# Performance work log

Hardware: AMD Instinct MI355X
Metric: run time of the kernel (lower is better)

Reference implementation:

```python
import jax, jax.numpy as jnp
import numpy as np

B, T, C, H = 8, 2048, 768, 768

def setup_inputs() -> dict:
    key = jax.random.key(0)
    ks = jax.random.split(key, 7)
    s = 1.0 / np.sqrt(C)
    return {
        "visual_token": jax.random.normal(ks[0], (B, T, C), dtype=jnp.float32),
        "Wk": jax.random.normal(ks[1], (H, C), dtype=jnp.float32) * s,
        "bk": jax.random.normal(ks[2], (H,), dtype=jnp.float32) * s,
        "Wq": jax.random.normal(ks[3], (H, C), dtype=jnp.float32) * s,
        "bq": jax.random.normal(ks[4], (H,), dtype=jnp.float32) * s,
        "W1": jax.random.normal(ks[5], (C, C), dtype=jnp.float32) * s,
        "W2": jax.random.normal(ks[6], (C, C), dtype=jnp.float32) * s,
    }

def reference(visual_token, Wk, bk, Wq, bq, W1, W2):
    x = visual_token
    k = jnp.einsum('btc,hc->bth', x, Wk) + bk          # [B,T,H]
    q = jnp.einsum('btc,hc->bth', x, Wq) + bq          # [B,T,H]
    scores = jnp.einsum('bih,bjh->bij', k, q)          # K @ Q^T, unscaled
    attn = jax.nn.softmax(scores, axis=1)              # NOTE: softmax over dim=1 as in source
    p = x + jnp.einsum('bij,bjc->bic', attn, x)        # residual with value = input
    h = jnp.einsum('btc,dc->btd', p, W1)               # f_1 (no bias)
    h = jnp.einsum('btd,ed->bte', h, W2)               # f_2 (no bias)
    return p + jax.nn.relu(h)
```

## Files before the change

kernel.cpp:

```cpp
#include <hip/hip_runtime.h>

typedef float    f32x4 __attribute__((ext_vector_type(4)));
typedef _Float16 f16x8 __attribute__((ext_vector_type(8)));
typedef _Float16 f16x4 __attribute__((ext_vector_type(4)));

__device__ __forceinline__ void gload16(const void* g, void* l) {
  __builtin_amdgcn_global_load_lds(
      (__attribute__((address_space(1))) void*)(const void*)g,
      (__attribute__((address_space(3))) void*)l,
      16, 0, 0);
}

template <int EPI>
__global__ __launch_bounds__(512, 4) void gemm_kt(
    const _Float16* __restrict__ A, size_t sA, int lda,
    const _Float16* __restrict__ B, size_t sB, int ldb,
    float* __restrict__ out0, _Float16* __restrict__ out1,
    float* __restrict__ out2,
    size_t sO, int ldo,
    const float* __restrict__ bias,
    const float* __restrict__ resid,
    const _Float16* __restrict__ residh,
    const _Float16* __restrict__ cf,
    int K) {
  __shared__ _Float16 lds[3 * 12288];
  __shared__ _Float16 clds[(EPI == 6) ? 4096 : 1];

  const int gx = gridDim.x, gy = gridDim.y;
  const int nblk = gx * gy * gridDim.z;
  int lin = (blockIdx.z * gy + blockIdx.y) * gx + blockIdx.x;
  lin = (lin & 7) * (nblk >> 3) + (lin >> 3);
  const int b  = lin / (gx * gy);
  const int r2 = lin - b * gx * gy;
  const int m0 = (r2 / gx) * 128;
  const int n0 = (r2 - (r2 / gx) * gx) * 256;

  const int t = threadIdx.x, lane = t & 63, w = t >> 6;
  const int wr = w >> 2;
  const int wc = w & 3;
  const int lr = lane & 15, lq = lane >> 4;

  const _Float16* Ab = A + (size_t)b * sA;
  const _Float16* Bb = B + (size_t)b * sB;

  const int arow = t >> 2;
  const int acol = ((t & 3) ^ ((arow >> 1) & 3)) * 8;
  const _Float16* a_src  = Ab + (size_t)(m0 + arow) * lda + acol;
  const _Float16* b_src0 = Bb + (size_t)(n0 + arow) * ldb + acol;
  const _Float16* b_src1 = b_src0 + (size_t)128 * ldb;
  const int a_dst  = t * 8;
  const int b_dst0 = 4096 + t * 8;
  const int b_dst1 = 4096 + (t + 512) * 8;

  const int swz  = ((lr >> 1) & 3) << 3;
  const int koff = (lq * 8) ^ swz;
  const int a_rd = (wr * 64 + lr) * 32 + koff;
  const int b_rd = 4096 + (wc * 64 + lr) * 32 + koff;

  f32x4 acc[4][4];
#pragma unroll
  for (int f = 0; f < 4; ++f)
#pragma unroll
    for (int j = 0; j < 4; ++j) acc[f][j] = (f32x4){0.f, 0.f, 0.f, 0.f};

  const int NT = K >> 5;

  if constexpr (EPI == 6)
    gload16(cf + ((size_t)b * 32 + (m0 >> 6)) * 2048 + t * 8, clds + t * 8);
  gload16(a_src,       lds + a_dst);
  gload16(b_src0,      lds + b_dst0);
  gload16(b_src1,      lds + b_dst1);
  gload16(a_src  + 32, lds + 12288 + a_dst);
  gload16(b_src0 + 32, lds + 12288 + b_dst0);
  gload16(b_src1 + 32, lds + 12288 + b_dst1);

  int buf = 0;
  for (int kt = 0; kt < NT; ++kt) {
    if (kt + 1 < NT) asm volatile("s_waitcnt vmcnt(3)" ::: "memory");
    else             asm volatile("s_waitcnt vmcnt(0)" ::: "memory");
    __builtin_amdgcn_s_barrier();
    __builtin_amdgcn_sched_barrier(0);

    const _Float16* lb = lds + buf * 12288;
    const int nb = (buf + 2 >= 3) ? buf - 1 : buf + 2;
    _Float16* ln = lds + nb * 12288;

    f16x8 af[4], bf[4], cv;
    if constexpr (EPI == 6)
      cv = *(const f16x8*)(clds + wr * 2048 + kt * 32 + lq * 8);
#pragma unroll
    for (int f = 0; f < 4; ++f) {
      af[f] = *(const f16x8*)(lb + a_rd + f * 512);
      if constexpr (EPI == 6) af[f] = af[f] * cv;
    }
#pragma unroll
    for (int j = 0; j < 4; ++j) bf[j] = *(const f16x8*)(lb + b_rd + j * 512);
    if (kt + 2 < NT) {
      const int ko = (kt + 2) * 32;
      gload16(a_src  + ko, ln + a_dst);
      gload16(b_src0 + ko, ln + b_dst0);
      gload16(b_src1 + ko, ln + b_dst1);
    }
    __builtin_amdgcn_s_setprio(1);
#pragma unroll
    for (int f = 0; f < 4; ++f)
#pragma unroll
      for (int j = 0; j < 4; ++j)
        acc[f][j] = __builtin_amdgcn_mfma_f32_16x16x32_f16(af[f], bf[j], acc[f][j], 0, 0, 0);
    __builtin_amdgcn_s_setprio(0);
    __builtin_amdgcn_sched_barrier(0);
    buf = (buf + 1 >= 3) ? 0 : buf + 1;
  }

  if constexpr (EPI == 4) {
#pragma unroll
    for (int j = 0; j < 4; ++j) {
      float m = -3.4e38f;
#pragma unroll
      for (int f = 0; f < 4; ++f)
#pragma unroll
        for (int r = 0; r < 4; ++r) m = fmaxf(m, acc[f][j][r]);
#pragma unroll
      for (int d = 16; d <= 32; d <<= 1) m = fmaxf(m, __shfl_xor(m, d, 64));
      float Z = 0.f;
      const int col = n0 + wc * 64 + j * 16 + lr;
#pragma unroll
      for (int f = 0; f < 4; ++f)
#pragma unroll
        for (int r = 0; r < 4; ++r) {
          const _Float16 eh = (_Float16)__expf(acc[f][j][r] - m);
          const int row = m0 + wr * 64 + f * 16 + lq * 4 + r;
          out1[(size_t)b * sO + (size_t)row * ldo + col] = eh;
          Z += (float)eh;
        }
#pragma unroll
      for (int d = 16; d <= 32; d <<= 1) Z += __shfl_xor(Z, d, 64);
      if (lq == 0) {
        const int chunk = (m0 >> 6) + wr;
        const size_t sidx = ((size_t)b * 32 + chunk) * 2048 + col;
        out0[sidx] = m;
        out2[sidx] = Z;
      }
    }
  } else {
#pragma unroll
    for (int f = 0; f < 4; ++f)
#pragma unroll
      for (int j = 0; j < 4; ++j)
#pragma unroll
        for (int r = 0; r < 4; ++r) {
          const int row = m0 + wr * 64 + f * 16 + lq * 4 + r;
          const int col = n0 + wc * 64 + j * 16 + lr;
          const size_t oidx = (size_t)b * sO + (size_t)row * ldo + col;
          float v = acc[f][j][r];
          if constexpr (EPI == 0) {
            if (bias) v += bias[col];
            out1[oidx] = (_Float16)v;
          } else if constexpr (EPI == 6) {
            out1[oidx] = (_Float16)(v + resid[oidx]);
          } else {
            out0[oidx] = (float)residh[oidx] + (v > 0.f ? v : 0.f);
          }
        }
  }
}

__global__ __launch_bounds__(256) void convert_f32_f16(const float* __restrict__ in,
                                                       _Float16* __restrict__ out, long n8) {
  long i = (long)blockIdx.x * blockDim.x + threadIdx.x;
  if (i >= n8) return;
  f32x4 v0 = *(const f32x4*)(in + i * 8);
  f32x4 v1 = *(const f32x4*)(in + i * 8 + 4);
  f16x8 o;
  o[0] = (_Float16)v0[0]; o[1] = (_Float16)v0[1]; o[2] = (_Float16)v0[2]; o[3] = (_Float16)v0[3];
  o[4] = (_Float16)v1[0]; o[5] = (_Float16)v1[1]; o[6] = (_Float16)v1[2]; o[7] = (_Float16)v1[3];
  *(f16x8*)(out + i * 8) = o;
}

__global__ void concat_bias(const float* __restrict__ bk, const float* __restrict__ bq,
                            float* __restrict__ bkq) {
  const int i = blockIdx.x * 256 + threadIdx.x;
  if (i < 768) bkq[i] = bk[i];
  else if (i < 1536) bkq[i] = bq[i - 768];
}

__global__ __launch_bounds__(256) void col_final(const float* __restrict__ pm,
                                                 const float* __restrict__ pZ,
                                                 _Float16* __restrict__ c) {
  const int b = blockIdx.z;
  const int col = blockIdx.x * 256 + threadIdx.x;
  float mv[32];
  float m = -3.4e38f;
#pragma unroll
  for (int k = 0; k < 32; ++k) {
    mv[k] = pm[((size_t)b * 32 + k) * 2048 + col];
    m = fmaxf(m, mv[k]);
  }
  float Z = 0.f;
#pragma unroll
  for (int k = 0; k < 32; ++k)
    Z += pZ[((size_t)b * 32 + k) * 2048 + col] * __expf(mv[k] - m);
  const float rZ = 1.f / Z;
#pragma unroll
  for (int k = 0; k < 32; ++k)
    c[((size_t)b * 32 + k) * 2048 + col] = (_Float16)(__expf(mv[k] - m) * rZ);
}

__global__ void xprep(const float* __restrict__ x, _Float16* __restrict__ xf,
                      _Float16* __restrict__ xT) {
  __shared__ float tile[32][33];
  const int b = blockIdx.z;
  const int c0 = blockIdx.x * 32, j0 = blockIdx.y * 32;
  const float* xb = x + (size_t)b * 2048 * 768;
  const int tx = threadIdx.x, ty = threadIdx.y;
#pragma unroll
  for (int dy = 0; dy < 32; dy += 8)
    tile[ty + dy][tx] = xb[(size_t)(j0 + ty + dy) * 768 + c0 + tx];
  __syncthreads();
  {
    const int u = ty * 32 + tx;
    const int row = u >> 3, c4 = (u & 7) * 4;
    f16x4 o;
#pragma unroll
    for (int q = 0; q < 4; ++q) o[q] = (_Float16)tile[row][c4 + q];
    *(f16x4*)(xf + ((size_t)b * 2048 + j0 + row) * 768 + c0 + c4) = o;
  }
  _Float16* xTb = xT + (size_t)b * 768 * 2048;
#pragma unroll
  for (int dy = 0; dy < 32; dy += 8)
    xTb[(size_t)(c0 + ty + dy) * 2048 + j0 + tx] = (_Float16)tile[tx][ty + dy];
}

extern "C" void kernel_launch(void* const* d_in, const int* in_sizes, int n_in,
                              void* d_out, int out_size, void* d_ws, size_t ws_size,
                              hipStream_t stream) {
  const float* x  = (const float*)d_in[0];
  const float* Wk = (const float*)d_in[1];
  const float* bk = (const float*)d_in[2];
  const float* Wq = (const float*)d_in[3];
  const float* bq = (const float*)d_in[4];
  const float* W1 = (const float*)d_in[5];
  const float* W2 = (const float*)d_in[6];
  float* out = (float*)d_out;

  char* ws = (char*)d_ws;
  size_t off = 0;
  auto alloc = [&](size_t bytes) -> char* {
    char* p = ws + off;
    off += (bytes + 255) & ~(size_t)255;
    return p;
  };
  _Float16* xf = (_Float16*)alloc(25165824);
  _Float16* kq = (_Float16*)alloc(50331648);
  _Float16* Wf = (_Float16*)alloc(4718592);
  _Float16* E  = (_Float16*)alloc(67108864);
  _Float16* xT = (_Float16*)alloc(25165824);
  float*    pm = (float*)alloc(2097152);
  float*    pZ = (float*)alloc(2097152);
  float*    bkq  = (float*)alloc(6144);

  _Float16* Wkqf = Wf;
  _Float16* W1f  = Wf + 2 * 589824;
  _Float16* W2f  = Wf + 3 * 589824;
  _Float16* pf16 = kq;
  _Float16* cT   = kq + 12582912;
  _Float16* hf16 = kq + 12582912;

  const size_t sKQ = (size_t)2048 * 1536;
  const size_t sS  = (size_t)2048 * 2048;
  const size_t sKV = (size_t)2048 * 768;

  xprep<<<dim3(24, 64, 8), dim3(32, 8), 0, stream>>>(x, xf, xT);
  convert_f32_f16<<<288, 256, 0, stream>>>(Wk, Wkqf, 73728);
  convert_f32_f16<<<288, 256, 0, stream>>>(Wq, Wkqf + 589824, 73728);
  convert_f32_f16<<<288, 256, 0, stream>>>(W1, W1f, 73728);
  convert_f32_f16<<<288, 256, 0, stream>>>(W2, W2f, 73728);
  concat_bias<<<6, 256, 0, stream>>>(bk, bq, bkq);

  gemm_kt<0><<<dim3(6, 128, 1), 512, 0, stream>>>(xf, 0, 768, Wkqf, 0, 768,
                                                  nullptr, kq, nullptr, 0, 1536,
                                                  bkq, nullptr, nullptr, nullptr, 768);

  gemm_kt<4><<<dim3(8, 16, 8), 512, 0, stream>>>(kq, sKQ, 1536, kq + 768, sKQ, 1536,
                                                 pm, E, pZ, sS, 2048,
                                                 nullptr, nullptr, nullptr, nullptr, 768);
  col_final<<<dim3(8, 1, 8), 256, 0, stream>>>(pm, pZ, cT);

  gemm_kt<6><<<dim3(3, 16, 8), 512, 0, stream>>>(E, sS, 2048, xT, sKV, 2048,
                                                 nullptr, pf16, nullptr, sKV, 768,
                                                 nullptr, x, nullptr, cT, 2048);

  gemm_kt<0><<<dim3(3, 128, 1), 512, 0, stream>>>(pf16, 0, 768, W1f, 0, 768,
                                                  nullptr, hf16, nullptr, 0, 768,
                                                  nullptr, nullptr, nullptr, nullptr, 768);

  gemm_kt<3><<<dim3(3, 128, 1), 512, 0, stream>>>(hf16, 0, 768, W2f, 0, 768,
                                                  out, nullptr, nullptr, 0, 768,
                                                  nullptr, nullptr, pf16, nullptr, 768);
}
```

Before: 282.9 us.

## Stage fp16 GEMM epilogue outputs through LDS for coalesced stores; merge weight conversion kernels

The fp16-output GEMM epilogues (bias, exp/softmax partials, residual add) now write each wave's tile into a swizzled LDS region and then flush it to global memory with 16-byte row-contiguous vector stores. This replaces scattered 2-byte per-element stores. Separately, the four weight conversions and the bias concat are merged into a single launch to cut launch overhead. The cost is two extra block barriers and an LDS round trip per tile, and the staging reuses the pipeline LDS buffers.

```diff
diff --git a/kernel.cpp b/kernel.cpp
--- a/kernel.cpp
+++ b/kernel.cpp
@@ -9,6 +9,20 @@
       (__attribute__((address_space(1))) void*)(const void*)g,
       (__attribute__((address_space(3))) void*)l,
       16, 0, 0);
+}
+
+__device__ __forceinline__ void bounce_flush(const _Float16* lds, _Float16* gbase,
+                                             int ldo, int t) {
+#pragma unroll
+  for (int it = 0; it < 8; ++it) {
+    const int s = t + it * 512;
+    const int R = s >> 5;
+    const int C = (s & 31) * 8;
+    const int wsrc = ((R >> 6) << 2) | (C >> 6);
+    const f16x8 v = *(const f16x8*)(lds + wsrc * 4096 + (R & 63) * 64 +
+                                    ((C & 63) ^ ((R & 12) << 2)));
+    *(f16x8*)(gbase + (size_t)R * ldo + C) = v;
+  }
 }
 
 template <int EPI>
@@ -112,36 +126,61 @@
     buf = (buf + 1 >= 3) ? 0 : buf + 1;
   }
 
-  if constexpr (EPI == 4) {
-#pragma unroll
-    for (int j = 0; j < 4; ++j) {
-      float m = -3.4e38f;
+  if constexpr (EPI == 0 || EPI == 4 || EPI == 6) {
+    __syncthreads();
+    _Float16* breg = lds + w * 4096;
+    if constexpr (EPI == 4) {
+#pragma unroll
+      for (int j = 0; j < 4; ++j) {
+        float m = -3.4e38f;
+#pragma unroll
+        for (int f = 0; f < 4; ++f)
+#pragma unroll
+          for (int r = 0; r < 4; ++r) m = fmaxf(m, acc[f][j][r]);
+#pragma unroll
+        for (int d = 16; d <= 32; d <<= 1) m = fmaxf(m, __shfl_xor(m, d, 64));
+        float Z = 0.f;
+        const int cb = ((j ^ lq) << 4) + lr;
+#pragma unroll
+        for (int f = 0; f < 4; ++f)
+#pragma unroll
+          for (int r = 0; r < 4; ++r) {
+            const _Float16 eh = (_Float16)__expf(acc[f][j][r] - m);
+            breg[(f * 16 + lq * 4 + r) * 64 + cb] = eh;
+            Z += (float)eh;
+          }
+#pragma unroll
+        for (int d = 16; d <= 32; d <<= 1) Z += __shfl_xor(Z, d, 64);
+        if (lq == 0) {
+          const int chunk = (m0 >> 6) + wr;
+          const int col = n0 + wc * 64 + j * 16 + lr;
+          const size_t sidx = ((size_t)b * 32 + chunk) * 2048 + col;
+          out0[sidx] = m;
+          out2[sidx] = Z;
+        }
+      }
+    } else {
 #pragma unroll
       for (int f = 0; f < 4; ++f)
 #pragma unroll
-        for (int r = 0; r < 4; ++r) m = fmaxf(m, acc[f][j][r]);
-#pragma unroll
-      for (int d = 16; d <= 32; d <<= 1) m = fmaxf(m, __shfl_xor(m, d, 64));
-      float Z = 0.f;
-      const int col = n0 + wc * 64 + j * 16 + lr;
-#pragma unroll
-      for (int f = 0; f < 4; ++f)
-#pragma unroll
-        for (int r = 0; r < 4; ++r) {
-          const _Float16 eh = (_Float16)__expf(acc[f][j][r] - m);
-          const int row = m0 + wr * 64 + f * 16 + lq * 4 + r;
-          out1[(size_t)b * sO + (size_t)row * ldo + col] = eh;
-          Z += (float)eh;
+        for (int j = 0; j < 4; ++j) {
+          const int cb = ((j ^ lq) << 4) + lr;
+#pragma unroll
+          for (int r = 0; r < 4; ++r) {
+            float v = acc[f][j][r];
+            if constexpr (EPI == 0) {
+              if (bias) v += bias[n0 + wc * 64 + j * 16 + lr];
+            } else {
+              const int row = m0 + wr * 64 + f * 16 + lq * 4 + r;
+              const int col = n0 + wc * 64 + j * 16 + lr;
+              v += resid[(size_t)b * sO + (size_t)row * ldo + col];
+            }
+            breg[(f * 16 + lq * 4 + r) * 64 + cb] = (_Float16)v;
+          }
         }
-#pragma unroll
-      for (int d = 16; d <= 32; d <<= 1) Z += __shfl_xor(Z, d, 64);
-      if (lq == 0) {
-        const int chunk = (m0 >> 6) + wr;
-        const size_t sidx = ((size_t)b * 32 + chunk) * 2048 + col;
-        out0[sidx] = m;
-        out2[sidx] = Z;
-      }
     }
+    __syncthreads();
+    bounce_flush(lds, out1 + (size_t)b * sO + (size_t)m0 * ldo + n0, ldo, t);
   } else {
 #pragma unroll
     for (int f = 0; f < 4; ++f)
@@ -152,36 +191,35 @@
           const int row = m0 + wr * 64 + f * 16 + lq * 4 + r;
           const int col = n0 + wc * 64 + j * 16 + lr;
           const size_t oidx = (size_t)b * sO + (size_t)row * ldo + col;
-          float v = acc[f][j][r];
-          if constexpr (EPI == 0) {
-            if (bias) v += bias[col];
-            out1[oidx] = (_Float16)v;
-          } else if constexpr (EPI == 6) {
-            out1[oidx] = (_Float16)(v + resid[oidx]);
-          } else {
-            out0[oidx] = (float)residh[oidx] + (v > 0.f ? v : 0.f);
-          }
+          const float v = acc[f][j][r];
+          out0[oidx] = (float)residh[oidx] + (v > 0.f ? v : 0.f);
         }
   }
 }
 
-__global__ __launch_bounds__(256) void convert_f32_f16(const float* __restrict__ in,
-                                                       _Float16* __restrict__ out, long n8) {
-  long i = (long)blockIdx.x * blockDim.x + threadIdx.x;
-  if (i >= n8) return;
+__global__ __launch_bounds__(256) void wconv(
+    const float* __restrict__ Wk, const float* __restrict__ Wq,
+    const float* __restrict__ W1, const float* __restrict__ W2,
+    _Float16* __restrict__ Wkqf, _Float16* __restrict__ W1f,
+    _Float16* __restrict__ W2f,
+    const float* __restrict__ bk, const float* __restrict__ bq,
+    float* __restrict__ bkq) {
+  const int by = blockIdx.y;
+  const long i = (long)blockIdx.x * 256 + threadIdx.x;
+  if (by == 4) {
+    if (i < 768) bkq[i] = bk[i];
+    else if (i < 1536) bkq[i] = bq[i - 768];
+    return;
+  }
+  const float* in = (by == 0) ? Wk : (by == 1) ? Wq : (by == 2) ? W1 : W2;
+  _Float16* outp = (by == 0) ? Wkqf : (by == 1) ? (Wkqf + 589824)
+                  : (by == 2) ? W1f : W2f;
   f32x4 v0 = *(const f32x4*)(in + i * 8);
   f32x4 v1 = *(const f32x4*)(in + i * 8 + 4);
   f16x8 o;
   o[0] = (_Float16)v0[0]; o[1] = (_Float16)v0[1]; o[2] = (_Float16)v0[2]; o[3] = (_Float16)v0[3];
   o[4] = (_Float16)v1[0]; o[5] = (_Float16)v1[1]; o[6] = (_Float16)v1[2]; o[7] = (_Float16)v1[3];
-  *(f16x8*)(out + i * 8) = o;
-}
-
-__global__ void concat_bias(const float* __restrict__ bk, const float* __restrict__ bq,
-                            float* __restrict__ bkq) {
-  const int i = blockIdx.x * 256 + threadIdx.x;
-  if (i < 768) bkq[i] = bk[i];
-  else if (i < 1536) bkq[i] = bq[i - 768];
+  *(f16x8*)(outp + i * 8) = o;
 }
 
 __global__ __launch_bounds__(256) void col_final(const float* __restrict__ pm,
@@ -271,11 +309,8 @@
   const size_t sKV = (size_t)2048 * 768;
 
   xprep<<<dim3(24, 64, 8), dim3(32, 8), 0, stream>>>(x, xf, xT);
-  convert_f32_f16<<<288, 256, 0, stream>>>(Wk, Wkqf, 73728);
-  convert_f32_f16<<<288, 256, 0, stream>>>(Wq, Wkqf + 589824, 73728);
-  convert_f32_f16<<<288, 256, 0, stream>>>(W1, W1f, 73728);
-  convert_f32_f16<<<288, 256, 0, stream>>>(W2, W2f, 73728);
-  concat_bias<<<6, 256, 0, stream>>>(bk, bq, bkq);
+  wconv<<<dim3(288, 5), 256, 0, stream>>>(Wk, Wq, W1, W2, Wkqf, W1f, W2f,
+                                          bk, bq, bkq);
 
   gemm_kt<0><<<dim3(6, 128, 1), 512, 0, stream>>>(xf, 0, 768, Wkqf, 0, 768,
                                                   nullptr, kq, nullptr, 0, 1536,
```

Result: faster. 264.0 us (median of 2 runs) (-6.7%).
